# Performance work log

Hardware: AMD Instinct MI355X
Metric: run time of the kernel (lower is better)

Reference implementation:

```python
import jax, jax.numpy as jnp
import numpy as np

N_NODES = 50000
N_EDGES = 800000
N_GRAPHS = 64
IN_CH = 128
HID_CH = 128
FC_CH = 128


def setup_inputs() -> dict:
    key = jax.random.key(0)
    ks = jax.random.split(key, 12)

    def lin_w(k, fan_in, fan_out):
        return jax.random.normal(k, (fan_in, fan_out), jnp.float32) * (1.0 / np.sqrt(fan_in))

    return {
        "x": jax.random.normal(ks[0], (N_NODES, IN_CH), jnp.float32),
        "edge_index": jax.random.randint(ks[1], (2, N_EDGES), 0, N_NODES, dtype=jnp.int64),
        "batch_vec": jnp.sort(jax.random.randint(ks[2], (N_NODES,), 0, N_GRAPHS, dtype=jnp.int64)),
        "W1": lin_w(ks[3], IN_CH, HID_CH),
        "b1": jnp.zeros((HID_CH,), jnp.float32),
        "W2": lin_w(ks[4], HID_CH, HID_CH),
        "b2": jnp.zeros((HID_CH,), jnp.float32),
        "W3": lin_w(ks[5], HID_CH, FC_CH),
        "b3": jnp.zeros((FC_CH,), jnp.float32),
        "fcW1": lin_w(ks[6], FC_CH, IN_CH),
        "fcb1": jnp.zeros((IN_CH,), jnp.float32),
        "fcW2": lin_w(ks[7], IN_CH, 2),
        "fcb2": jnp.zeros((2,), jnp.float32),
    }


def reference(x, edge_index, batch_vec, W1, b1, W2, b2, W3, b3, fcW1, fcb1, fcW2, fcb2):
    n = x.shape[0]
    row, col = edge_index[0], edge_index[1]  # src -> dst

    # GCN symmetric normalization with self-loops: deg[j] = in-degree(j) + 1
    deg = jnp.zeros((n,), x.dtype).at[col].add(1.0) + 1.0
    inv_sqrt = jax.lax.rsqrt(deg)
    edge_norm = inv_sqrt[row] * inv_sqrt[col]  # [E]
    self_norm = (inv_sqrt * inv_sqrt)[:, None]  # [N,1], self-loop weight 1/deg

    def gcn(h, W, b):
        h = h @ W  # [N, out]
        agg = jnp.zeros_like(h).at[col].add(h[row] * edge_norm[:, None])
        return agg + h * self_norm + b

    h = jax.nn.relu(gcn(x, W1, b1))
    h = jax.nn.relu(gcn(h, W2, b2))
    h = jax.nn.relu(gcn(h, W3, b3))
    h = jax.nn.relu(h @ fcW1 + fcb1)
    h = h @ fcW2 + fcb2  # [N, 2]

    # global mean pool per graph
    sums = jax.ops.segment_sum(h, batch_vec, num_segments=N_GRAPHS)
    cnts = jax.ops.segment_sum(jnp.ones((n,), h.dtype), batch_vec, num_segments=N_GRAPHS)
    pooled = sums / jnp.maximum(cnts, 1.0)[:, None]  # [G, 2]
    return jax.nn.softmax(pooled, axis=1)
```

## Files before the change

### kernel.cpp

```cpp
#include <hip/hip_runtime.h>


#define CH 128
#define BSH 7
#define SEG 4096
#define SEGP 5120
#define EPW 2048
#define SAF 136
#define SC8 144

typedef unsigned short ushortT;
typedef unsigned int uintT;
typedef unsigned char ucharT;
typedef __attribute__((ext_vector_type(8))) short short8;
typedef __attribute__((ext_vector_type(4))) float floatx4;
typedef __attribute__((ext_vector_type(2))) float floatx2;

__device__ __forceinline__ float bf2f(uintT u) {
    return __uint_as_float(u << 16);
}
__device__ __forceinline__ ushortT f2bf(float f) {
    uintT x = __float_as_uint(f);
    return (ushortT)((x + 0x7fffu + ((x >> 16) & 1u)) >> 16);
}
__device__ __forceinline__ void dec4p(uintT u, floatx2& lo, floatx2& hi) {
    lo = __builtin_amdgcn_cvt_pk_f32_fp8((int)u, false);
    hi = __builtin_amdgcn_cvt_pk_f32_fp8((int)u, true);
}
__device__ __forceinline__ uintT packbf(floatx2 v) {
    return __builtin_amdgcn_perm(__float_as_uint(v.y), __float_as_uint(v.x), 0x07060302u);
}

__global__ __launch_bounds__(256) void k_bin(const int* __restrict__ row,
                                             const int* __restrict__ col,
                                             int* __restrict__ bfill,
                                             uintT* __restrict__ seg,
                                             const float* __restrict__ X,
                                             ucharT* __restrict__ Xb,
                                             const float* __restrict__ w0,
                                             const float* __restrict__ w1,
                                             const float* __restrict__ w2,
                                             const float* __restrict__ w3,
                                             ushortT* __restrict__ Whi,
                                             float* __restrict__ sums,
                                             int* __restrict__ tdone,
                                             int E, int NBB, int NB, int G,
                                             int total4) {
    __shared__ uintT staged[EPW];
    __shared__ int target[EPW];
    __shared__ int sval[512];
    __shared__ int horig[512];
    __shared__ int pcnt[512];
    __shared__ int gbase[512];
    const int t = threadIdx.x;

    if ((int)blockIdx.x >= NBB) {
        int bb = (int)blockIdx.x - NBB;
        if (bb < 256) {
            int idx = bb * 256 + t;
            int m = idx >> 14;
            int r2 = idx & 16383;
            int n = r2 >> 7;
            int k = r2 & 127;
            const float* W = (m == 0) ? w0 : (m == 1) ? w1 : (m == 2) ? w2 : w3;
            Whi[m * 16384 + n * CH + k] = f2bf(W[k * CH + n]);
            if (bb == 0) {
                if (t < 3 * G) sums[t] = 0.f;
                if (t == 0) tdone[0] = 0;
            }
        } else {
            int i = (bb - 256) * 256 + t;
            if (i < total4) {
                float4 v = reinterpret_cast<const float4*>(X)[i];
                int r0 = __builtin_amdgcn_cvt_pk_fp8_f32(v.x, v.y, 0, false);
                int r1 = __builtin_amdgcn_cvt_pk_fp8_f32(v.z, v.w, r0, true);
                reinterpret_cast<int*>(Xb)[i] = r1;
            }
        }
        return;
    }

    const int e0 = blockIdx.x * EPW;
    const int cnt = min(EPW, E - e0);

    sval[t] = 0; sval[t + 256] = 0;
    __syncthreads();

    int er[8], ec[8];
#pragma unroll
    for (int i = 0; i < 8; ++i) {
        int le = i * 256 + t;
        if (le < cnt) {
            er[i] = row[e0 + le];
            ec[i] = col[e0 + le];
            atomicAdd(&sval[ec[i] >> BSH], 1);
        }
    }
    __syncthreads();
    horig[t] = sval[t]; horig[t + 256] = sval[t + 256];
    __syncthreads();
    for (int off = 1; off < 512; off <<= 1) {
        int a = (t >= off) ? sval[t - off] : 0;
        int b2 = sval[t + 256 - off];
        __syncthreads();
        sval[t] += a;
        sval[t + 256] += b2;
        __syncthreads();
    }
    for (int b = t; b < 512; b += 256) {
        int h = horig[b];
        pcnt[b] = sval[b] - h;
        gbase[b] = (h > 0 && b < NB) ? atomicAdd(&bfill[b], h) : 0;
    }
    __syncthreads();
#pragma unroll
    for (int i = 0; i < 8; ++i) {
        int le = i * 256 + t;
        if (le < cnt) {
            int b = ec[i] >> BSH;
            int j = atomicAdd(&pcnt[b], 1);
            staged[j] = (uintT)er[i] | ((uintT)ec[i] << 16);
            int lo = sval[b] - horig[b];
            target[j] = b * SEG + gbase[b] + (j - lo);
        }
    }
    __syncthreads();
    for (int s = t; s < cnt; s += 256) seg[target[s]] = staged[s];
}

__global__ __launch_bounds__(512) void k_binvs(const int* __restrict__ bfill,
                                               const uintT* __restrict__ seg,
                                               float* __restrict__ invs,
                                               int* __restrict__ degi,
                                               int NB, int N) {
    const int b = blockIdx.x;
    const int t = threadIdx.x;
    __shared__ int h[128];
    if (t < 128) h[t] = 0;
    __syncthreads();
    int cnt = bfill[b];
    const uintT* sp = seg + (size_t)b * SEG;
    for (int s = t; s < cnt; s += 512) atomicAdd(&h[(sp[s] >> 16) & 127], 1);
    __syncthreads();
    int d = b * 128 + t;
    if (t < 128 && d < N) {
        invs[d] = rsqrtf((float)h[t] + 1.0f);
        degi[d] = h[t];
    }
}

__global__ __launch_bounds__(256) void k_scatter(const int* __restrict__ bfill,
                                                 const uintT* __restrict__ seg,
                                                 const float* __restrict__ invs,
                                                 const int* __restrict__ degi,
                                                 uintT* __restrict__ indptr,
                                                 uintT* __restrict__ epack,
                                                 int N, int NB) {
    __shared__ __align__(16) uintT staged[SEGP];
    __shared__ int pinc[128];
    __shared__ int pc[128];
    __shared__ float invL[128];
    __shared__ int ptotS;
    const int t = threadIdx.x;
    const int b = blockIdx.x;
    const int cnt = bfill[b];
    const uintT* sp = seg + (size_t)b * SEG;

    int praw = 0, hp = 0;
    if (t < 128) {
        int d = b * 128 + t;
        praw = (d < N) ? degi[d] : 0;
        invL[t] = (d < N) ? invs[d] : 0.f;
        hp = (praw + 7) & ~7;
        pinc[t] = hp;
    }
    __syncthreads();
    for (int off = 1; off < 128; off <<= 1) {
        int a = (t >= off && t < 128) ? pinc[t - off] : 0;
        __syncthreads();
        if (t < 128) pinc[t] += a;
        __syncthreads();
    }
    int excl = 0;
    if (t < 128) {
        excl = pinc[t] - hp;
        pc[t] = excl;
        int d = b * 128 + t;
        if (d < N) indptr[d] = (uintT)(b * SEGP + excl) | ((uintT)(hp >> 3) << 21);
        if (t == 127) ptotS = pinc[127];
    }
    __syncthreads();
    for (int s = t; s < cnt; s += 256) {
        uintT rc = sp[s];
        int src = (int)(rc & 0xffffu);
        int d7 = (int)(rc >> 16) & 127;
        int j = atomicAdd(&pc[d7], 1);
        float nrm = invs[src] * invL[d7];
        staged[j] = (uintT)src | ((uintT)f2bf(nrm) << 16);
    }
    __syncthreads();
    if (t < 128) {
        for (int k = excl + praw; k < excl + hp; ++k) staged[k] = 0u;
    }
    __syncthreads();
    {
        int tot4 = ptotS >> 2;
        uint4* dstw = reinterpret_cast<uint4*>(epack + (size_t)b * SEGP);
        const uint4* srcw = reinterpret_cast<const uint4*>(staged);
        for (int s = t; s < tot4; s += 256) dstw[s] = srcw[s];
    }
}

__global__ __launch_bounds__(256, 6) void k_agg(const ucharT* __restrict__ H8,
                                                const uintT* __restrict__ epack,
                                                const uintT* __restrict__ indptr,
                                                const float* __restrict__ invs,
                                                ucharT* __restrict__ Z8, int N) {
    const int wave = threadIdx.x >> 6, lane = threadIdx.x & 63;
    const int ng = lane >> 3;
    const int l = lane & 7;
    const int node = blockIdx.x * 32 + wave * 8 + ng;
    if (node >= N) return;

    const uint4* H4 = reinterpret_cast<const uint4*>(H8);
    const uint4* E4 = reinterpret_cast<const uint4*>(epack);

    uintT v = indptr[node];
    int q0 = (int)(v & 0x1FFFFFu) >> 2;
    int nb = (int)(v >> 21);

    floatx2 acc2[8];
    {
        float sn = invs[node];
        float sn2 = sn * sn;
        floatx2 s2 = {sn2, sn2};
        uint4 hrow = H4[(size_t)node * 8 + l];
        uintT wd[4] = {hrow.x, hrow.y, hrow.z, hrow.w};
#pragma unroll
        for (int w = 0; w < 4; ++w) {
            floatx2 lo, hi;
            dec4p(wd[w], lo, hi);
            acc2[2 * w] = s2 * lo;
            acc2[2 * w + 1] = s2 * hi;
        }
    }

    auto proc = [&](uint4 ea, uint4 eb) {
        uintT rec[8] = {ea.x, ea.y, ea.z, ea.w, eb.x, eb.y, eb.z, eb.w};
        uint4 g[8];
#pragma unroll
        for (int i = 0; i < 8; ++i)
            g[i] = H4[(size_t)(int)(rec[i] & 0xffffu) * 8 + l];
#pragma unroll
        for (int i = 0; i < 8; ++i) {
            float wv = bf2f(rec[i] >> 16);
            floatx2 wv2 = {wv, wv};
            uintT wd[4] = {g[i].x, g[i].y, g[i].z, g[i].w};
#pragma unroll
            for (int w = 0; w < 4; ++w) {
                floatx2 lo, hi;
                dec4p(wd[w], lo, hi);
                acc2[2 * w] += wv2 * lo;
                acc2[2 * w + 1] += wv2 * hi;
            }
        }
    };

    if (nb > 0) {
        uint4 ea = E4[q0], eb = E4[q0 + 1];
        for (int it = 1; it < nb; ++it) {
            uint4 na = E4[q0 + 2 * it], nbv = E4[q0 + 2 * it + 1];
            proc(ea, eb);
            ea = na; eb = nbv;
        }
        proc(ea, eb);
    }

    uint4 o;
    {
        int r0 = __builtin_amdgcn_cvt_pk_fp8_f32(acc2[0].x, acc2[0].y, 0, false);
        r0 = __builtin_amdgcn_cvt_pk_fp8_f32(acc2[1].x, acc2[1].y, r0, true);
        int r1 = __builtin_amdgcn_cvt_pk_fp8_f32(acc2[2].x, acc2[2].y, 0, false);
        r1 = __builtin_amdgcn_cvt_pk_fp8_f32(acc2[3].x, acc2[3].y, r1, true);
        int r2 = __builtin_amdgcn_cvt_pk_fp8_f32(acc2[4].x, acc2[4].y, 0, false);
        r2 = __builtin_amdgcn_cvt_pk_fp8_f32(acc2[5].x, acc2[5].y, r2, true);
        int r3 = __builtin_amdgcn_cvt_pk_fp8_f32(acc2[6].x, acc2[6].y, 0, false);
        r3 = __builtin_amdgcn_cvt_pk_fp8_f32(acc2[7].x, acc2[7].y, r3, true);
        o.x = (uintT)r0; o.y = (uintT)r1; o.z = (uintT)r2; o.w = (uintT)r3;
    }
    reinterpret_cast<uint4*>(Z8)[(size_t)node * 8 + l] = o;
}

__global__ __launch_bounds__(256) void k_gemm(const ucharT* __restrict__ In8,
                                              const ushortT* __restrict__ Whi,
                                              const float* __restrict__ Bias,
                                              ucharT* __restrict__ Out8, int N) {
    __shared__ ushortT As[64 * SAF];
    __shared__ ushortT Ws[128 * SAF];

    const int tid = threadIdx.x;
    const int wave = tid >> 6, lane = tid & 63;
    const int quad = lane >> 4, l15 = lane & 15;
    const int mBase = (wave >> 1) * 32, nBase = (wave & 1) * 64;
    const int row0 = blockIdx.x * 64;
    const int r = tid >> 2, q = tid & 3;

    {
        int grow = row0 + r;
        uint4 a8 = {0, 0, 0, 0}, b8 = {0, 0, 0, 0};
        if (grow < N) {
            const uint4* s = reinterpret_cast<const uint4*>(In8 + (size_t)grow * CH + q * 32);
            a8 = s[0]; b8 = s[1];
        }
        uintT wds[8] = {a8.x, a8.y, a8.z, a8.w, b8.x, b8.y, b8.z, b8.w};
#pragma unroll
        for (int w = 0; w < 4; ++w) {
            floatx2 lo0, hi0, lo1, hi1;
            dec4p(wds[2 * w], lo0, hi0);
            dec4p(wds[2 * w + 1], lo1, hi1);
            uint4 o;
            o.x = packbf(lo0); o.y = packbf(hi0);
            o.z = packbf(lo1); o.w = packbf(hi1);
            *reinterpret_cast<uint4*>(&As[r * SAF + q * 32 + w * 8]) = o;
        }
        int wn = tid & 127, wh = tid >> 7;
        const uint4* sh = reinterpret_cast<const uint4*>(Whi + wn * CH + wh * 64);
        uint4* dh = reinterpret_cast<uint4*>(&Ws[wn * SAF + wh * 64]);
#pragma unroll
        for (int p = 0; p < 8; ++p) dh[p] = sh[p];
    }
    __syncthreads();

    floatx4 acc[2][4];
    const floatx4 zero4 = {0.f, 0.f, 0.f, 0.f};
#pragma unroll
    for (int i = 0; i < 2; i++)
#pragma unroll
        for (int j = 0; j < 4; j++) acc[i][j] = zero4;

#pragma unroll
    for (int ks = 0; ks < 4; ++ks) {
        short8 af[2], wf[4];
#pragma unroll
        for (int mt = 0; mt < 2; ++mt)
            af[mt] = *reinterpret_cast<const short8*>(&As[(mBase + mt * 16 + l15) * SAF + ks * 32 + quad * 8]);
#pragma unroll
        for (int nt = 0; nt < 4; ++nt)
            wf[nt] = *reinterpret_cast<const short8*>(&Ws[(nBase + nt * 16 + l15) * SAF + ks * 32 + quad * 8]);
#pragma unroll
        for (int mt = 0; mt < 2; ++mt)
#pragma unroll
            for (int nt = 0; nt < 4; ++nt)
                acc[mt][nt] = __builtin_amdgcn_mfma_f32_16x16x32_bf16(af[mt], wf[nt], acc[mt][nt], 0, 0, 0);
    }
    __syncthreads();

    float bb[4];
#pragma unroll
    for (int nt = 0; nt < 4; ++nt) bb[nt] = Bias[nBase + nt * 16 + l15];

    ucharT* Cs8 = reinterpret_cast<ucharT*>(As);
#pragma unroll
    for (int mt = 0; mt < 2; ++mt)
#pragma unroll
        for (int nt = 0; nt < 4; ++nt)
#pragma unroll
            for (int r4 = 0; r4 < 4; ++r4) {
                int lrow = mBase + mt * 16 + quad * 4 + r4;
                float v = fmaxf(acc[mt][nt][r4] + bb[nt], 0.f);
                int f8 = __builtin_amdgcn_cvt_pk_fp8_f32(v, 0.f, 0, false);
                Cs8[lrow * SC8 + nBase + nt * 16 + l15] = (ucharT)(f8 & 0xff);
            }
    __syncthreads();
    {
        int grow = row0 + r;
        if (grow < N) {
            const uint4* s4 = reinterpret_cast<const uint4*>(&Cs8[r * SC8 + q * 32]);
            uint4* dst = reinterpret_cast<uint4*>(Out8 + (size_t)grow * CH + q * 32);
            dst[0] = s4[0];
            dst[1] = s4[1];
        }
    }
}

__global__ __launch_bounds__(256) void k_tail(const ucharT* __restrict__ Z8,
                                              const ushortT* __restrict__ W3hi,
                                              const float* __restrict__ B3,
                                              const ushortT* __restrict__ F1hi,
                                              const float* __restrict__ FB1,
                                              const float* __restrict__ FW2,
                                              const float* __restrict__ FB2,
                                              const int* __restrict__ batch,
                                              float* __restrict__ sums,
                                              float* __restrict__ cnts,
                                              float* __restrict__ out,
                                              int* __restrict__ tdone,
                                              int N, int G) {
    __shared__ ushortT Hf[64 * SAF];
    __shared__ ushortT Ws[128 * SAF];
    __shared__ float rp0[128];
    __shared__ float rp1[128];
    __shared__ float ls[192];
    __shared__ int lastFlag;

    const int tid = threadIdx.x;
    const int wave = tid >> 6, lane = tid & 63;
    const int quad = lane >> 4, l15 = lane & 15;
    const int mBase = (wave >> 1) * 32, nBase = (wave & 1) * 64;
    const int row0 = blockIdx.x * 64;
    const int r = tid >> 2, q = tid & 3;
    const int wn = tid & 127, wh = tid >> 7;

    {
        int grow = row0 + r;
        uint4 a8 = {0, 0, 0, 0}, b8 = {0, 0, 0, 0};
        if (grow < N) {
            const uint4* s = reinterpret_cast<const uint4*>(Z8 + (size_t)grow * CH + q * 32);
            a8 = s[0]; b8 = s[1];
        }
        uintT wds[8] = {a8.x, a8.y, a8.z, a8.w, b8.x, b8.y, b8.z, b8.w};
#pragma unroll
        for (int w = 0; w < 4; ++w) {
            floatx2 lo0, hi0, lo1, hi1;
            dec4p(wds[2 * w], lo0, hi0);
            dec4p(wds[2 * w + 1], lo1, hi1);
            uint4 o;
            o.x = packbf(lo0); o.y = packbf(hi0);
            o.z = packbf(lo1); o.w = packbf(hi1);
            *reinterpret_cast<uint4*>(&Hf[r * SAF + q * 32 + w * 8]) = o;
        }
        const uint4* sh = reinterpret_cast<const uint4*>(W3hi + wn * CH + wh * 64);
        uint4* dh = reinterpret_cast<uint4*>(&Ws[wn * SAF + wh * 64]);
#pragma unroll
        for (int p = 0; p < 8; ++p) dh[p] = sh[p];
    }
    __syncthreads();

    floatx4 acc[2][4];
    const floatx4 zero4 = {0.f, 0.f, 0.f, 0.f};
#pragma unroll
    for (int i = 0; i < 2; i++)
#pragma unroll
        for (int j = 0; j < 4; j++) acc[i][j] = zero4;

#pragma unroll
    for (int ks = 0; ks < 4; ++ks) {
        short8 af[2], wf[4];
#pragma unroll
        for (int mt = 0; mt < 2; ++mt)
            af[mt] = *reinterpret_cast<const short8*>(&Hf[(mBase + mt * 16 + l15) * SAF + ks * 32 + quad * 8]);
#pragma unroll
        for (int nt = 0; nt < 4; ++nt)
            wf[nt] = *reinterpret_cast<const short8*>(&Ws[(nBase + nt * 16 + l15) * SAF + ks * 32 + quad * 8]);
#pragma unroll
        for (int mt = 0; mt < 2; ++mt)
#pragma unroll
            for (int nt = 0; nt < 4; ++nt)
                acc[mt][nt] = __builtin_amdgcn_mfma_f32_16x16x32_bf16(af[mt], wf[nt], acc[mt][nt], 0, 0, 0);
    }
    __syncthreads();

    {
        float bb[4];
#pragma unroll
        for (int nt = 0; nt < 4; ++nt) bb[nt] = B3[nBase + nt * 16 + l15];
#pragma unroll
        for (int mt = 0; mt < 2; ++mt)
#pragma unroll
            for (int nt = 0; nt < 4; ++nt)
#pragma unroll
                for (int r4 = 0; r4 < 4; ++r4) {
                    int lrow = mBase + mt * 16 + quad * 4 + r4;
                    float v = fmaxf(acc[mt][nt][r4] + bb[nt], 0.f);
                    Hf[lrow * SAF + nBase + nt * 16 + l15] = f2bf(v);
                }
        const uint4* sh = reinterpret_cast<const uint4*>(F1hi + wn * CH + wh * 64);
        uint4* dh = reinterpret_cast<uint4*>(&Ws[wn * SAF + wh * 64]);
#pragma unroll
        for (int p = 0; p < 8; ++p) dh[p] = sh[p];
    }
    __syncthreads();

#pragma unroll
    for (int i = 0; i < 2; i++)
#pragma unroll
        for (int j = 0; j < 4; j++) acc[i][j] = zero4;
#pragma unroll
    for (int ks = 0; ks < 4; ++ks) {
        short8 af[2], wf[4];
#pragma unroll
        for (int mt = 0; mt < 2; ++mt)
            af[mt] = *reinterpret_cast<const short8*>(&Hf[(mBase + mt * 16 + l15) * SAF + ks * 32 + quad * 8]);
#pragma unroll
        for (int nt = 0; nt < 4; ++nt)
            wf[nt] = *reinterpret_cast<const short8*>(&Ws[(nBase + nt * 16 + l15) * SAF + ks * 32 + quad * 8]);
#pragma unroll
        for (int mt = 0; mt < 2; ++mt)
#pragma unroll
            for (int nt = 0; nt < 4; ++nt)
                acc[mt][nt] = __builtin_amdgcn_mfma_f32_16x16x32_bf16(af[mt], wf[nt], acc[mt][nt], 0, 0, 0);
    }

    {
        float bb[4];
#pragma unroll
        for (int nt = 0; nt < 4; ++nt) bb[nt] = FB1[nBase + nt * 16 + l15];
        float w20[4], w21[4];
#pragma unroll
        for (int nt = 0; nt < 4; ++nt) {
            float2 wv = *reinterpret_cast<const float2*>(FW2 + 2 * (nBase + nt * 16 + l15));
            w20[nt] = wv.x;
            w21[nt] = wv.y;
        }
#pragma unroll
        for (int mt = 0; mt < 2; ++mt)
#pragma unroll
            for (int r4 = 0; r4 < 4; ++r4) {
                float d0 = 0.f, d1 = 0.f;
#pragma unroll
                for (int nt = 0; nt < 4; ++nt) {
                    float v = fmaxf(acc[mt][nt][r4] + bb[nt], 0.f);
                    d0 += v * w20[nt];
                    d1 += v * w21[nt];
                }
#pragma unroll
                for (int m = 8; m >= 1; m >>= 1) {
                    d0 += __shfl_xor(d0, m, 64);
                    d1 += __shfl_xor(d1, m, 64);
                }
                if (l15 == 0) {
                    int lrow = mBase + mt * 16 + quad * 4 + r4;
                    rp0[lrow * 2 + (wave & 1)] = d0;
                    rp1[lrow * 2 + (wave & 1)] = d1;
                }
            }
    }
    if (tid < 192) ls[tid] = 0.f;
    __syncthreads();

    if (tid < 64) {
        int node = row0 + tid;
        if (node < N) {
            float d0 = rp0[tid * 2] + rp0[tid * 2 + 1] + FB2[0];
            float d1 = rp1[tid * 2] + rp1[tid * 2 + 1] + FB2[1];
            int g = batch[node];
            atomicAdd(&ls[g], d0);
            atomicAdd(&ls[64 + g], d1);
            atomicAdd(&ls[128 + g], 1.0f);
        }
    }
    __syncthreads();
    if (tid < 64) {
        float c = ls[128 + tid];
        if (c != 0.f) {
            atomicAdd(&sums[2 * tid], ls[tid]);
            atomicAdd(&sums[2 * tid + 1], ls[64 + tid]);
            atomicAdd(&cnts[tid], c);
        }
    }
    __syncthreads();

    if (tid == 0) {
        int old = atomicAdd(tdone, 1);
        lastFlag = (old == (int)gridDim.x - 1) ? 1 : 0;
    }
    __syncthreads();
    if (lastFlag && tid < G) {
        int g = tid;
        float c = fmaxf(atomicAdd(&cnts[g], 0.f), 1.0f);
        float p0 = atomicAdd(&sums[2 * g], 0.f) / c;
        float p1 = atomicAdd(&sums[2 * g + 1], 0.f) / c;
        float m = fmaxf(p0, p1);
        float e0 = expf(p0 - m), e1 = expf(p1 - m);
        float inv = 1.f / (e0 + e1);
        out[2 * g] = e0 * inv;
        out[2 * g + 1] = e1 * inv;
    }
}

extern "C" void kernel_launch(void* const* d_in, const int* in_sizes, int n_in,
                              void* d_out, int out_size, void* d_ws, size_t ws_size,
                              hipStream_t stream) {
    const float* X   = (const float*)d_in[0];
    const int* EI    = (const int*)d_in[1];
    const int* BATCH = (const int*)d_in[2];
    const float* W1  = (const float*)d_in[3];
    const float* B1  = (const float*)d_in[4];
    const float* W2  = (const float*)d_in[5];
    const float* B2  = (const float*)d_in[6];
    const float* W3  = (const float*)d_in[7];
    const float* B3  = (const float*)d_in[8];
    const float* FW1 = (const float*)d_in[9];
    const float* FB1 = (const float*)d_in[10];
    const float* FW2 = (const float*)d_in[11];
    const float* FB2 = (const float*)d_in[12];

    const int N = in_sizes[0] / CH;
    const int E = in_sizes[1] / 2;
    const int G = out_size / 2;
    const int* rowp = EI;
    const int* colp = EI + E;
    const int NB = (N + 127) >> BSH;

    char* w = (char*)d_ws;
    auto alloc = [&](size_t bytes) -> char* {
        char* p = w;
        w += (bytes + 255) & ~(size_t)255;
        return p;
    };
    ucharT*  Z8    = (ucharT*)alloc((size_t)N * CH);
    ucharT*  Hb8   = (ucharT*)alloc((size_t)N * CH);
    ucharT*  Xb8   = (ucharT*)alloc((size_t)N * CH);
    ushortT* WhiA  = (ushortT*)alloc((size_t)4 * 16384 * 2);
    float* invs    = (float*)alloc((size_t)N * 4);
    int*   degi    = (int*)alloc((size_t)N * 4);
    uintT* indptr  = (uintT*)alloc((size_t)N * 4);
    uintT* epack   = (uintT*)alloc((size_t)NB * SEGP * 4);
    uintT* seg     = (uintT*)alloc((size_t)NB * SEG * 4);
    int*   bfill   = (int*)alloc((size_t)NB * 4);
    float* sums    = (float*)alloc((size_t)G * 3 * 4);
    float* cnts    = sums + 2 * G;
    int*   tdone   = (int*)alloc(256);

    const int nbAgg  = (N + 31) / 32;
    const int nbGemm = (N + 63) / 64;
    const int nbBin  = (E + EPW - 1) / EPW;
    const int total4 = N * CH / 4;
    const int nbXc   = (total4 + 255) / 256;

    hipMemsetAsync(bfill, 0, (size_t)NB * 4, stream);
    k_bin<<<nbBin + 256 + nbXc, 256, 0, stream>>>(rowp, colp, bfill, seg,
                                                  X, Xb8, W1, W2, W3, FW1, WhiA,
                                                  sums, tdone, E, nbBin, NB, G, total4);
    k_binvs<<<NB, 512, 0, stream>>>(bfill, seg, invs, degi, NB, N);
    k_scatter<<<NB, 256, 0, stream>>>(bfill, seg, invs, degi, indptr, epack, N, NB);

    k_agg<<<nbAgg, 256, 0, stream>>>(Xb8, epack, indptr, invs, Z8, N);
    k_gemm<<<nbGemm, 256, 0, stream>>>(Z8, WhiA, B1, Hb8, N);
    k_agg<<<nbAgg, 256, 0, stream>>>(Hb8, epack, indptr, invs, Z8, N);
    k_gemm<<<nbGemm, 256, 0, stream>>>(Z8, WhiA + 16384, B2, Hb8, N);
    k_agg<<<nbAgg, 256, 0, stream>>>(Hb8, epack, indptr, invs, Z8, N);
    k_tail<<<nbGemm, 256, 0, stream>>>(Z8, WhiA + 2 * 16384, B3,
                                       WhiA + 3 * 16384, FB1, FW2, FB2,
                                       BATCH, sums, cnts, (float*)d_out, tdone, N, G);
}
```

Before: 213.6 us.

## Fuse all GCN stages into one persistent cooperative kernel with grid syncs

Replaces the chain of separate kernel launches (binning, degree, scatter, three aggregations, two GEMMs, tail) with a single cooperative persistent kernel. Each phase loops over its tasks with a grid-stride loop and is separated from the next by grid.sync(). The intent is to remove per-launch gaps and the last-block counter used for the softmax. The trade-offs are that the grid is capped by occupancy (at most 2048 blocks), so each phase gets fewer resident blocks, and the aggregation loses its launch_bounds(256,6) occupancy hint. A fallback path of multiple kernels is kept in case cooperative launch sizing fails.

After: 550.2 us. 158% more time.

```diff
diff --git a/kernel.cpp b/kernel.cpp
--- a/kernel.cpp
+++ b/kernel.cpp
@@ -1,4 +1,7 @@
 #include <hip/hip_runtime.h>
+#include <hip/hip_cooperative_groups.h>
+
+namespace cg = cooperative_groups;
 
 
 #define CH 128
@@ -8,6 +11,7 @@
 #define EPW 2048
 #define SAF 136
 #define SC8 144
+#define SMEM_BYTES 24576
 
 typedef unsigned short ushortT;
 typedef unsigned int uintT;
@@ -31,616 +35,639 @@
     return __builtin_amdgcn_perm(__float_as_uint(v.y), __float_as_uint(v.x), 0x07060302u);
 }
 
-__global__ __launch_bounds__(256) void k_bin(const int* __restrict__ row,
-                                             const int* __restrict__ col,
-                                             int* __restrict__ bfill,
-                                             uintT* __restrict__ seg,
-                                             const float* __restrict__ X,
-                                             ucharT* __restrict__ Xb,
-                                             const float* __restrict__ w0,
-                                             const float* __restrict__ w1,
-                                             const float* __restrict__ w2,
-                                             const float* __restrict__ w3,
-                                             ushortT* __restrict__ Whi,
-                                             float* __restrict__ sums,
-                                             int* __restrict__ tdone,
-                                             int E, int NBB, int NB, int G,
-                                             int total4) {
-    __shared__ uintT staged[EPW];
-    __shared__ int target[EPW];
-    __shared__ int sval[512];
-    __shared__ int horig[512];
-    __shared__ int pcnt[512];
-    __shared__ int gbase[512];
+struct MP {
+    const int* rowp; const int* colp; const int* batch;
+    const float* X;
+    const float *W1, *B1, *W2, *B2, *W3, *B3, *FW1, *FB1, *FW2, *FB2;
+    ucharT *Z8, *Hb8, *Xb8;
+    ushortT* Whi;
+    float* invs; int* degi;
+    uintT *indptr, *epack, *seg;
+    int* bfill;
+    float* sums; float* cnts;
+    float* out;
+    int N, E, G, NB, nbBin, nbAgg, nbG, total4, nbX16;
+};
+
+__device__ __forceinline__ void ph_prep(const MP& p, unsigned char* smem) {
     const int t = threadIdx.x;
-
-    if ((int)blockIdx.x >= NBB) {
-        int bb = (int)blockIdx.x - NBB;
-        if (bb < 256) {
+    const int T0 = p.nbBin + 256 + p.nbX16;
+    for (int task = blockIdx.x; task < T0; task += gridDim.x) {
+        if (task < p.nbBin) {
+            uintT* staged = (uintT*)smem;
+            int* target = (int*)(smem + 8192);
+            int* sval  = (int*)(smem + 16384);
+            int* horig = (int*)(smem + 18432);
+            int* pcnt  = (int*)(smem + 20480);
+            int* gbase = (int*)(smem + 22528);
+            const int e0 = task * EPW;
+            const int cnt = min(EPW, p.E - e0);
+            sval[t] = 0; sval[t + 256] = 0;
+            __syncthreads();
+            int er[8], ec[8];
+#pragma unroll
+            for (int i = 0; i < 8; ++i) {
+                int le = i * 256 + t;
+                if (le < cnt) {
+                    er[i] = p.rowp[e0 + le];
+                    ec[i] = p.colp[e0 + le];
+                    atomicAdd(&sval[ec[i] >> BSH], 1);
+                }
+            }
+            __syncthreads();
+            horig[t] = sval[t]; horig[t + 256] = sval[t + 256];
+            __syncthreads();
+            for (int off = 1; off < 512; off <<= 1) {
+                int a = (t >= off) ? sval[t - off] : 0;
+                int b2 = sval[t + 256 - off];
+                __syncthreads();
+                sval[t] += a;
+                sval[t + 256] += b2;
+                __syncthreads();
+            }
+            for (int b = t; b < 512; b += 256) {
+                int h = horig[b];
+                pcnt[b] = sval[b] - h;
+                gbase[b] = (h > 0 && b < p.NB) ? atomicAdd(&p.bfill[b], h) : 0;
+            }
+            __syncthreads();
+#pragma unroll
+            for (int i = 0; i < 8; ++i) {
+                int le = i * 256 + t;
+                if (le < cnt) {
+                    int b = ec[i] >> BSH;
+                    int j = atomicAdd(&pcnt[b], 1);
+                    staged[j] = (uintT)er[i] | ((uintT)ec[i] << 16);
+                    int lo = sval[b] - horig[b];
+                    target[j] = b * SEG + gbase[b] + (j - lo);
+                }
+            }
+            __syncthreads();
+            for (int s = t; s < cnt; s += 256) p.seg[target[s]] = staged[s];
+            __syncthreads();
+        } else if (task < p.nbBin + 256) {
+            int bb = task - p.nbBin;
             int idx = bb * 256 + t;
             int m = idx >> 14;
             int r2 = idx & 16383;
             int n = r2 >> 7;
             int k = r2 & 127;
-            const float* W = (m == 0) ? w0 : (m == 1) ? w1 : (m == 2) ? w2 : w3;
-            Whi[m * 16384 + n * CH + k] = f2bf(W[k * CH + n]);
-            if (bb == 0) {
-                if (t < 3 * G) sums[t] = 0.f;
-                if (t == 0) tdone[0] = 0;
-            }
+            const float* W = (m == 0) ? p.W1 : (m == 1) ? p.W2 : (m == 2) ? p.W3 : p.FW1;
+            p.Whi[m * 16384 + n * CH + k] = f2bf(W[k * CH + n]);
+            if (bb == 0 && t < 3 * p.G) p.sums[t] = 0.f;
         } else {
-            int i = (bb - 256) * 256 + t;
-            if (i < total4) {
-                float4 v = reinterpret_cast<const float4*>(X)[i];
-                int r0 = __builtin_amdgcn_cvt_pk_fp8_f32(v.x, v.y, 0, false);
-                int r1 = __builtin_amdgcn_cvt_pk_fp8_f32(v.z, v.w, r0, true);
-                reinterpret_cast<int*>(Xb)[i] = r1;
-            }
-        }
-        return;
-    }
-
-    const int e0 = blockIdx.x * EPW;
-    const int cnt = min(EPW, E - e0);
-
-    sval[t] = 0; sval[t + 256] = 0;
-    __syncthreads();
-
-    int er[8], ec[8];
-#pragma unroll
-    for (int i = 0; i < 8; ++i) {
-        int le = i * 256 + t;
-        if (le < cnt) {
-            er[i] = row[e0 + le];
-            ec[i] = col[e0 + le];
-            atomicAdd(&sval[ec[i] >> BSH], 1);
-        }
-    }
-    __syncthreads();
-    horig[t] = sval[t]; horig[t + 256] = sval[t + 256];
-    __syncthreads();
-    for (int off = 1; off < 512; off <<= 1) {
-        int a = (t >= off) ? sval[t - off] : 0;
-        int b2 = sval[t + 256 - off];
-        __syncthreads();
-        sval[t] += a;
-        sval[t + 256] += b2;
-        __syncthreads();
-    }
-    for (int b = t; b < 512; b += 256) {
-        int h = horig[b];
-        pcnt[b] = sval[b] - h;
-        gbase[b] = (h > 0 && b < NB) ? atomicAdd(&bfill[b], h) : 0;
-    }
-    __syncthreads();
-#pragma unroll
-    for (int i = 0; i < 8; ++i) {
-        int le = i * 256 + t;
-        if (le < cnt) {
-            int b = ec[i] >> BSH;
-            int j = atomicAdd(&pcnt[b], 1);
-            staged[j] = (uintT)er[i] | ((uintT)ec[i] << 16);
-            int lo = sval[b] - horig[b];
-            target[j] = b * SEG + gbase[b] + (j - lo);
-        }
-    }
-    __syncthreads();
-    for (int s = t; s < cnt; s += 256) seg[target[s]] = staged[s];
-}
-
-__global__ __launch_bounds__(512) void k_binvs(const int* __restrict__ bfill,
-                                               const uintT* __restrict__ seg,
-                                               float* __restrict__ invs,
-                                               int* __restrict__ degi,
-                                               int NB, int N) {
-    const int b = blockIdx.x;
+            int xb = task - p.nbBin - 256;
+            int base = xb * 4096;
+#pragma unroll
+            for (int k = 0; k < 16; ++k) {
+                int i = base + k * 256 + t;
+                if (i < p.total4) {
+                    float4 v = reinterpret_cast<const float4*>(p.X)[i];
+                    int r0 = __builtin_amdgcn_cvt_pk_fp8_f32(v.x, v.y, 0, false);
+                    int r1 = __builtin_amdgcn_cvt_pk_fp8_f32(v.z, v.w, r0, true);
+                    reinterpret_cast<int*>(p.Xb8)[i] = r1;
+                }
+            }
+        }
+    }
+}
+
+__device__ __forceinline__ void ph_binvs(const MP& p, unsigned char* smem) {
     const int t = threadIdx.x;
-    __shared__ int h[128];
-    if (t < 128) h[t] = 0;
-    __syncthreads();
-    int cnt = bfill[b];
-    const uintT* sp = seg + (size_t)b * SEG;
-    for (int s = t; s < cnt; s += 512) atomicAdd(&h[(sp[s] >> 16) & 127], 1);
-    __syncthreads();
-    int d = b * 128 + t;
-    if (t < 128 && d < N) {
-        invs[d] = rsqrtf((float)h[t] + 1.0f);
-        degi[d] = h[t];
-    }
-}
-
-__global__ __launch_bounds__(256) void k_scatter(const int* __restrict__ bfill,
-                                                 const uintT* __restrict__ seg,
-                                                 const float* __restrict__ invs,
-                                                 const int* __restrict__ degi,
-                                                 uintT* __restrict__ indptr,
-                                                 uintT* __restrict__ epack,
-                                                 int N, int NB) {
-    __shared__ __align__(16) uintT staged[SEGP];
-    __shared__ int pinc[128];
-    __shared__ int pc[128];
-    __shared__ float invL[128];
-    __shared__ int ptotS;
+    int* h = (int*)smem;
+    for (int b = blockIdx.x; b < p.NB; b += gridDim.x) {
+        if (t < 128) h[t] = 0;
+        __syncthreads();
+        int cnt = p.bfill[b];
+        const uintT* sp = p.seg + (size_t)b * SEG;
+        for (int s = t; s < cnt; s += 256) atomicAdd(&h[(sp[s] >> 16) & 127], 1);
+        __syncthreads();
+        int d = b * 128 + t;
+        if (t < 128 && d < p.N) {
+            p.invs[d] = rsqrtf((float)h[t] + 1.0f);
+            p.degi[d] = h[t];
+        }
+        __syncthreads();
+    }
+}
+
+__device__ __forceinline__ void ph_scatter(const MP& p, unsigned char* smem) {
     const int t = threadIdx.x;
-    const int b = blockIdx.x;
-    const int cnt = bfill[b];
-    const uintT* sp = seg + (size_t)b * SEG;
-
-    int praw = 0, hp = 0;
-    if (t < 128) {
-        int d = b * 128 + t;
-        praw = (d < N) ? degi[d] : 0;
-        invL[t] = (d < N) ? invs[d] : 0.f;
-        hp = (praw + 7) & ~7;
-        pinc[t] = hp;
-    }
-    __syncthreads();
-    for (int off = 1; off < 128; off <<= 1) {
-        int a = (t >= off && t < 128) ? pinc[t - off] : 0;
-        __syncthreads();
-        if (t < 128) pinc[t] += a;
-        __syncthreads();
-    }
-    int excl = 0;
-    if (t < 128) {
-        excl = pinc[t] - hp;
-        pc[t] = excl;
-        int d = b * 128 + t;
-        if (d < N) indptr[d] = (uintT)(b * SEGP + excl) | ((uintT)(hp >> 3) << 21);
-        if (t == 127) ptotS = pinc[127];
-    }
-    __syncthreads();
-    for (int s = t; s < cnt; s += 256) {
-        uintT rc = sp[s];
-        int src = (int)(rc & 0xffffu);
-        int d7 = (int)(rc >> 16) & 127;
-        int j = atomicAdd(&pc[d7], 1);
-        float nrm = invs[src] * invL[d7];
-        staged[j] = (uintT)src | ((uintT)f2bf(nrm) << 16);
-    }
-    __syncthreads();
-    if (t < 128) {
-        for (int k = excl + praw; k < excl + hp; ++k) staged[k] = 0u;
-    }
-    __syncthreads();
-    {
-        int tot4 = ptotS >> 2;
-        uint4* dstw = reinterpret_cast<uint4*>(epack + (size_t)b * SEGP);
-        const uint4* srcw = reinterpret_cast<const uint4*>(staged);
-        for (int s = t; s < tot4; s += 256) dstw[s] = srcw[s];
-    }
-}
-
-__global__ __launch_bounds__(256, 6) void k_agg(const ucharT* __restrict__ H8,
-                                                const uintT* __restrict__ epack,
-                                                const uintT* __restrict__ indptr,
-                                                const float* __restrict__ invs,
-                                                ucharT* __restrict__ Z8, int N) {
+    uintT* staged = (uintT*)smem;
+    int* pinc = (int*)(smem + 20480);
+    int* pc   = (int*)(smem + 20992);
+    float* invL = (float*)(smem + 21504);
+    int* ptotS = (int*)(smem + 22016);
+    for (int b = blockIdx.x; b < p.NB; b += gridDim.x) {
+        const int cnt = p.bfill[b];
+        const uintT* sp = p.seg + (size_t)b * SEG;
+        int praw = 0, hp = 0;
+        if (t < 128) {
+            int d = b * 128 + t;
+            praw = (d < p.N) ? p.degi[d] : 0;
+            invL[t] = (d < p.N) ? p.invs[d] : 0.f;
+            hp = (praw + 7) & ~7;
+            pinc[t] = hp;
+        }
+        __syncthreads();
+        for (int off = 1; off < 128; off <<= 1) {
+            int a = (t >= off && t < 128) ? pinc[t - off] : 0;
+            __syncthreads();
+            if (t < 128) pinc[t] += a;
+            __syncthreads();
+        }
+        int excl = 0;
+        if (t < 128) {
+            excl = pinc[t] - hp;
+            pc[t] = excl;
+            int d = b * 128 + t;
+            if (d < p.N) p.indptr[d] = (uintT)(b * SEGP + excl) | ((uintT)(hp >> 3) << 21);
+            if (t == 127) ptotS[0] = pinc[127];
+        }
+        __syncthreads();
+        for (int s = t; s < cnt; s += 256) {
+            uintT rc = sp[s];
+            int src = (int)(rc & 0xffffu);
+            int d7 = (int)(rc >> 16) & 127;
+            int j = atomicAdd(&pc[d7], 1);
+            float nrm = p.invs[src] * invL[d7];
+            staged[j] = (uintT)src | ((uintT)f2bf(nrm) << 16);
+        }
+        __syncthreads();
+        if (t < 128) {
+            for (int k = excl + praw; k < excl + hp; ++k) staged[k] = 0u;
+        }
+        __syncthreads();
+        {
+            int tot4 = ptotS[0] >> 2;
+            uint4* dstw = reinterpret_cast<uint4*>(p.epack + (size_t)b * SEGP);
+            const uint4* srcw = reinterpret_cast<const uint4*>(staged);
+            for (int s = t; s < tot4; s += 256) dstw[s] = srcw[s];
+        }
+        __syncthreads();
+    }
+}
+
+__device__ __forceinline__ void ph_agg(const MP& p, const ucharT* H8, ucharT* Z8) {
     const int wave = threadIdx.x >> 6, lane = threadIdx.x & 63;
     const int ng = lane >> 3;
     const int l = lane & 7;
-    const int node = blockIdx.x * 32 + wave * 8 + ng;
-    if (node >= N) return;
-
     const uint4* H4 = reinterpret_cast<const uint4*>(H8);
-    const uint4* E4 = reinterpret_cast<const uint4*>(epack);
-
-    uintT v = indptr[node];
-    int q0 = (int)(v & 0x1FFFFFu) >> 2;
-    int nb = (int)(v >> 21);
-
-    floatx2 acc2[8];
-    {
-        float sn = invs[node];
-        float sn2 = sn * sn;
-        floatx2 s2 = {sn2, sn2};
-        uint4 hrow = H4[(size_t)node * 8 + l];
-        uintT wd[4] = {hrow.x, hrow.y, hrow.z, hrow.w};
-#pragma unroll
-        for (int w = 0; w < 4; ++w) {
-            floatx2 lo, hi;
-            dec4p(wd[w], lo, hi);
-            acc2[2 * w] = s2 * lo;
-            acc2[2 * w + 1] = s2 * hi;
-        }
-    }
-
-    auto proc = [&](uint4 ea, uint4 eb) {
-        uintT rec[8] = {ea.x, ea.y, ea.z, ea.w, eb.x, eb.y, eb.z, eb.w};
-        uint4 g[8];
-#pragma unroll
-        for (int i = 0; i < 8; ++i)
-            g[i] = H4[(size_t)(int)(rec[i] & 0xffffu) * 8 + l];
-#pragma unroll
-        for (int i = 0; i < 8; ++i) {
-            float wv = bf2f(rec[i] >> 16);
-            floatx2 wv2 = {wv, wv};
-            uintT wd[4] = {g[i].x, g[i].y, g[i].z, g[i].w};
-#pragma unroll
-            for (int w = 0; w < 4; ++w) {
-                floatx2 lo, hi;
-                dec4p(wd[w], lo, hi);
-                acc2[2 * w] += wv2 * lo;
-                acc2[2 * w + 1] += wv2 * hi;
-            }
-        }
-    };
-
-    if (nb > 0) {
-        uint4 ea = E4[q0], eb = E4[q0 + 1];
-        for (int it = 1; it < nb; ++it) {
-            uint4 na = E4[q0 + 2 * it], nbv = E4[q0 + 2 * it + 1];
-            proc(ea, eb);
-            ea = na; eb = nbv;
-        }
-        proc(ea, eb);
-    }
-
-    uint4 o;
-    {
-        int r0 = __builtin_amdgcn_cvt_pk_fp8_f32(acc2[0].x, acc2[0].y, 0, false);
-        r0 = __builtin_amdgcn_cvt_pk_fp8_f32(acc2[1].x, acc2[1].y, r0, true);
-        int r1 = __builtin_amdgcn_cvt_pk_fp8_f32(acc2[2].x, acc2[2].y, 0, false);
-        r1 = __builtin_amdgcn_cvt_pk_fp8_f32(acc2[3].x, acc2[3].y, r1, true);
-        int r2 = __builtin_amdgcn_cvt_pk_fp8_f32(acc2[4].x, acc2[4].y, 0, false);
-        r2 = __builtin_amdgcn_cvt_pk_fp8_f32(acc2[5].x, acc2[5].y, r2, true);
-        int r3 = __builtin_amdgcn_cvt_pk_fp8_f32(acc2[6].x, acc2[6].y, 0, false);
-        r3 = __builtin_amdgcn_cvt_pk_fp8_f32(acc2[7].x, acc2[7].y, r3, true);
-        o.x = (uintT)r0; o.y = (uintT)r1; o.z = (uintT)r2; o.w = (uintT)r3;
-    }
-    reinterpret_cast<uint4*>(Z8)[(size_t)node * 8 + l] = o;
-}
-
-__global__ __launch_bounds__(256) void k_gemm(const ucharT* __restrict__ In8,
-                                              const ushortT* __restrict__ Whi,
-                                              const float* __restrict__ Bias,
-                                              ucharT* __restrict__ Out8, int N) {
-    __shared__ ushortT As[64 * SAF];
-    __shared__ ushortT Ws[128 * SAF];
-
+    const uint4* E4 = reinterpret_cast<const uint4*>(p.epack);
+
+    for (int task = blockIdx.x; task < p.nbAgg; task += gridDim.x) {
+        const int node = task * 32 + wave * 8 + ng;
+        if (node < p.N) {
+            uintT v = p.indptr[node];
+            int q0 = (int)(v & 0x1FFFFFu) >> 2;
+            int nb = (int)(v >> 21);
+
+            floatx2 acc2[8];
+            {
+                float sn = p.invs[node];
+                float sn2 = sn * sn;
+                floatx2 s2 = {sn2, sn2};
+                uint4 hrow = H4[(size_t)node * 8 + l];
+                uintT wd[4] = {hrow.x, hrow.y, hrow.z, hrow.w};
+#pragma unroll
+                for (int w = 0; w < 4; ++w) {
+                    floatx2 lo, hi;
+                    dec4p(wd[w], lo, hi);
+                    acc2[2 * w] = s2 * lo;
+                    acc2[2 * w + 1] = s2 * hi;
+                }
+            }
+
+            auto proc = [&](uint4 ea, uint4 eb) {
+                uintT rec[8] = {ea.x, ea.y, ea.z, ea.w, eb.x, eb.y, eb.z, eb.w};
+                uint4 g[8];
+#pragma unroll
+                for (int i = 0; i < 8; ++i)
+                    g[i] = H4[(size_t)(int)(rec[i] & 0xffffu) * 8 + l];
+#pragma unroll
+                for (int i = 0; i < 8; ++i) {
+                    float wv = bf2f(rec[i] >> 16);
+                    floatx2 wv2 = {wv, wv};
+                    uintT wd[4] = {g[i].x, g[i].y, g[i].z, g[i].w};
+#pragma unroll
+                    for (int w = 0; w < 4; ++w) {
+                        floatx2 lo, hi;
+                        dec4p(wd[w], lo, hi);
+                        acc2[2 * w] += wv2 * lo;
+                        acc2[2 * w + 1] += wv2 * hi;
+                    }
+                }
+            };
+
+            if (nb > 0) {
+                uint4 ea = E4[q0], eb = E4[q0 + 1];
+                for (int it = 1; it < nb; ++it) {
+                    uint4 na = E4[q0 + 2 * it], nbv = E4[q0 + 2 * it + 1];
+                    proc(ea, eb);
+                    ea = na; eb = nbv;
+                }
+                proc(ea, eb);
+            }
+
+            uint4 o;
+            {
+                int r0 = __builtin_amdgcn_cvt_pk_fp8_f32(acc2[0].x, acc2[0].y, 0, false);
+                r0 = __builtin_amdgcn_cvt_pk_fp8_f32(acc2[1].x, acc2[1].y, r0, true);
+                int r1 = __builtin_amdgcn_cvt_pk_fp8_f32(acc2[2].x, acc2[2].y, 0, false);
+                r1 = __builtin_amdgcn_cvt_pk_fp8_f32(acc2[3].x, acc2[3].y, r1, true);
+                int r2 = __builtin_amdgcn_cvt_pk_fp8_f32(acc2[4].x, acc2[4].y, 0, false);
+                r2 = __builtin_amdgcn_cvt_pk_fp8_f32(acc2[5].x, acc2[5].y, r2, true);
+                int r3 = __builtin_amdgcn_cvt_pk_fp8_f32(acc2[6].x, acc2[6].y, 0, false);
+                r3 = __builtin_amdgcn_cvt_pk_fp8_f32(acc2[7].x, acc2[7].y, r3, true);
+                o.x = (uintT)r0; o.y = (uintT)r1; o.z = (uintT)r2; o.w = (uintT)r3;
+            }
+            reinterpret_cast<uint4*>(Z8)[(size_t)node * 8 + l] = o;
+        }
+    }
+}
+
+__device__ __forceinline__ void ph_gemm(const MP& p, const ucharT* In8,
+                                        const ushortT* Whi, const float* Bias,
+                                        ucharT* Out8, unsigned char* smem) {
+    ushortT* As = (ushortT*)smem;
     const int tid = threadIdx.x;
     const int wave = tid >> 6, lane = tid & 63;
     const int quad = lane >> 4, l15 = lane & 15;
     const int mBase = (wave >> 1) * 32, nBase = (wave & 1) * 64;
-    const int row0 = blockIdx.x * 64;
     const int r = tid >> 2, q = tid & 3;
 
-    {
-        int grow = row0 + r;
-        uint4 a8 = {0, 0, 0, 0}, b8 = {0, 0, 0, 0};
-        if (grow < N) {
-            const uint4* s = reinterpret_cast<const uint4*>(In8 + (size_t)grow * CH + q * 32);
-            a8 = s[0]; b8 = s[1];
-        }
-        uintT wds[8] = {a8.x, a8.y, a8.z, a8.w, b8.x, b8.y, b8.z, b8.w};
-#pragma unroll
-        for (int w = 0; w < 4; ++w) {
-            floatx2 lo0, hi0, lo1, hi1;
-            dec4p(wds[2 * w], lo0, hi0);
-            dec4p(wds[2 * w + 1], lo1, hi1);
-            uint4 o;
-            o.x = packbf(lo0); o.y = packbf(hi0);
-            o.z = packbf(lo1); o.w = packbf(hi1);
-            *reinterpret_cast<uint4*>(&As[r * SAF + q * 32 + w * 8]) = o;
-        }
-        int wn = tid & 127, wh = tid >> 7;
-        const uint4* sh = reinterpret_cast<const uint4*>(Whi + wn * CH + wh * 64);
-        uint4* dh = reinterpret_cast<uint4*>(&Ws[wn * SAF + wh * 64]);
-#pragma unroll
-        for (int p = 0; p < 8; ++p) dh[p] = sh[p];
-    }
-    __syncthreads();
-
-    floatx4 acc[2][4];
-    const floatx4 zero4 = {0.f, 0.f, 0.f, 0.f};
-#pragma unroll
-    for (int i = 0; i < 2; i++)
-#pragma unroll
-        for (int j = 0; j < 4; j++) acc[i][j] = zero4;
-
-#pragma unroll
-    for (int ks = 0; ks < 4; ++ks) {
-        short8 af[2], wf[4];
+    for (int task = blockIdx.x; task < p.nbG; task += gridDim.x) {
+        const int row0 = task * 64;
+        {
+            int grow = row0 + r;
+            uint4 a8 = {0, 0, 0, 0}, b8 = {0, 0, 0, 0};
+            if (grow < p.N) {
+                const uint4* s = reinterpret_cast<const uint4*>(In8 + (size_t)grow * CH + q * 32);
+                a8 = s[0]; b8 = s[1];
+            }
+            uintT wds[8] = {a8.x, a8.y, a8.z, a8.w, b8.x, b8.y, b8.z, b8.w};
+#pragma unroll
+            for (int w = 0; w < 4; ++w) {
+                floatx2 lo0, hi0, lo1, hi1;
+                dec4p(wds[2 * w], lo0, hi0);
+                dec4p(wds[2 * w + 1], lo1, hi1);
+                uint4 o;
+                o.x = packbf(lo0); o.y = packbf(hi0);
+                o.z = packbf(lo1); o.w = packbf(hi1);
+                *reinterpret_cast<uint4*>(&As[r * SAF + q * 32 + w * 8]) = o;
+            }
+        }
+        __syncthreads();
+
+        floatx4 acc[2][4];
+        const floatx4 zero4 = {0.f, 0.f, 0.f, 0.f};
+#pragma unroll
+        for (int i = 0; i < 2; i++)
+#pragma unroll
+            for (int j = 0; j < 4; j++) acc[i][j] = zero4;
+
+#pragma unroll
+        for (int ks = 0; ks < 4; ++ks) {
+            short8 af[2], wf[4];
+#pragma unroll
+            for (int mt = 0; mt < 2; ++mt)
+                af[mt] = *reinterpret_cast<const short8*>(&As[(mBase + mt * 16 + l15) * SAF + ks * 32 + quad * 8]);
+#pragma unroll
+            for (int nt = 0; nt < 4; ++nt)
+                wf[nt] = *reinterpret_cast<const short8*>(Whi + (size_t)(nBase + nt * 16 + l15) * CH + ks * 32 + quad * 8);
+#pragma unroll
+            for (int mt = 0; mt < 2; ++mt)
+#pragma unroll
+                for (int nt = 0; nt < 4; ++nt)
+                    acc[mt][nt] = __builtin_amdgcn_mfma_f32_16x16x32_bf16(af[mt], wf[nt], acc[mt][nt], 0, 0, 0);
+        }
+        __syncthreads();
+
+        float bb[4];
+#pragma unroll
+        for (int nt = 0; nt < 4; ++nt) bb[nt] = Bias[nBase + nt * 16 + l15];
+
+        ucharT* Cs8 = reinterpret_cast<ucharT*>(As);
 #pragma unroll
         for (int mt = 0; mt < 2; ++mt)
-            af[mt] = *reinterpret_cast<const short8*>(&As[(mBase + mt * 16 + l15) * SAF + ks * 32 + quad * 8]);
-#pragma unroll
-        for (int nt = 0; nt < 4; ++nt)
-            wf[nt] = *reinterpret_cast<const short8*>(&Ws[(nBase + nt * 16 + l15) * SAF + ks * 32 + quad * 8]);
-#pragma unroll
-        for (int mt = 0; mt < 2; ++mt)
 #pragma unroll
             for (int nt = 0; nt < 4; ++nt)
-                acc[mt][nt] = __builtin_amdgcn_mfma_f32_16x16x32_bf16(af[mt], wf[nt], acc[mt][nt], 0, 0, 0);
-    }
-    __syncthreads();
-
-    float bb[4];
-#pragma unroll
-    for (int nt = 0; nt < 4; ++nt) bb[nt] = Bias[nBase + nt * 16 + l15];
-
-    ucharT* Cs8 = reinterpret_cast<ucharT*>(As);
-#pragma unroll
-    for (int mt = 0; mt < 2; ++mt)
-#pragma unroll
-        for (int nt = 0; nt < 4; ++nt)
-#pragma unroll
-            for (int r4 = 0; r4 < 4; ++r4) {
-                int lrow = mBase + mt * 16 + quad * 4 + r4;
-                float v = fmaxf(acc[mt][nt][r4] + bb[nt], 0.f);
-                int f8 = __builtin_amdgcn_cvt_pk_fp8_f32(v, 0.f, 0, false);
-                Cs8[lrow * SC8 + nBase + nt * 16 + l15] = (ucharT)(f8 & 0xff);
-            }
-    __syncthreads();
-    {
-        int grow = row0 + r;
-        if (grow < N) {
-            const uint4* s4 = reinterpret_cast<const uint4*>(&Cs8[r * SC8 + q * 32]);
-            uint4* dst = reinterpret_cast<uint4*>(Out8 + (size_t)grow * CH + q * 32);
-            dst[0] = s4[0];
-            dst[1] = s4[1];
-        }
-    }
-}
-
-__global__ __launch_bounds__(256) void k_tail(const ucharT* __restrict__ Z8,
-                                              const ushortT* __restrict__ W3hi,
-                                              const float* __restrict__ B3,
-                                              const ushortT* __restrict__ F1hi,
-                                              const float* __restrict__ FB1,
-                                              const float* __restrict__ FW2,
-                                              const float* __restrict__ FB2,
-                                              const int* __restrict__ batch,
-                                              float* __restrict__ sums,
-                                              float* __restrict__ cnts,
-                                              float* __restrict__ out,
-                                              int* __restrict__ tdone,
-                                              int N, int G) {
-    __shared__ ushortT Hf[64 * SAF];
-    __shared__ ushortT Ws[128 * SAF];
-    __shared__ float rp0[128];
-    __shared__ float rp1[128];
-    __shared__ float ls[192];
-    __shared__ int lastFlag;
+#pragma unroll
+                for (int r4 = 0; r4 < 4; ++r4) {
+                    int lrow = mBase + mt * 16 + quad * 4 + r4;
+                    float v = fmaxf(acc[mt][nt][r4] + bb[nt], 0.f);
+                    int f8 = __builtin_amdgcn_cvt_pk_fp8_f32(v, 0.f, 0, false);
+                    Cs8[lrow * SC8 + nBase + nt * 16 + l15] = (ucharT)(f8 & 0xff);
+                }
+        __syncthreads();
+        {
+            int grow = row0 + r;
+            if (grow < p.N) {
+                const uint4* s4 = reinterpret_cast<const uint4*>(&Cs8[r * SC8 + q * 32]);
+                uint4* dst = reinterpret_cast<uint4*>(Out8 + (size_t)grow * CH + q * 32);
+                dst[0] = s4[0];
+                dst[1] = s4[1];
+            }
+        }
+        __syncthreads();
+    }
+}
+
+__device__ __forceinline__ void ph_tail(const MP& p, unsigned char* smem) {
+    ushortT* Hf = (ushortT*)smem;
+    float* rp0 = (float*)(smem + 17408);
+    float* rp1 = (float*)(smem + 17920);
+    float* ls  = (float*)(smem + 18432);
+    const ushortT* W3hi = p.Whi + 2 * 16384;
+    const ushortT* F1hi = p.Whi + 3 * 16384;
 
     const int tid = threadIdx.x;
     const int wave = tid >> 6, lane = tid & 63;
     const int quad = lane >> 4, l15 = lane & 15;
     const int mBase = (wave >> 1) * 32, nBase = (wave & 1) * 64;
-    const int row0 = blockIdx.x * 64;
     const int r = tid >> 2, q = tid & 3;
-    const int wn = tid & 127, wh = tid >> 7;
-
-    {
-        int grow = row0 + r;
-        uint4 a8 = {0, 0, 0, 0}, b8 = {0, 0, 0, 0};
-        if (grow < N) {
-            const uint4* s = reinterpret_cast<const uint4*>(Z8 + (size_t)grow * CH + q * 32);
-            a8 = s[0]; b8 = s[1];
-        }
-        uintT wds[8] = {a8.x, a8.y, a8.z, a8.w, b8.x, b8.y, b8.z, b8.w};
-#pragma unroll
-        for (int w = 0; w < 4; ++w) {
-            floatx2 lo0, hi0, lo1, hi1;
-            dec4p(wds[2 * w], lo0, hi0);
-            dec4p(wds[2 * w + 1], lo1, hi1);
-            uint4 o;
-            o.x = packbf(lo0); o.y = packbf(hi0);
-            o.z = packbf(lo1); o.w = packbf(hi1);
-            *reinterpret_cast<uint4*>(&Hf[r * SAF + q * 32 + w * 8]) = o;
-        }
-        const uint4* sh = reinterpret_cast<const uint4*>(W3hi + wn * CH + wh * 64);
-        uint4* dh = reinterpret_cast<uint4*>(&Ws[wn * SAF + wh * 64]);
-#pragma unroll
-        for (int p = 0; p < 8; ++p) dh[p] = sh[p];
-    }
-    __syncthreads();
-
-    floatx4 acc[2][4];
-    const floatx4 zero4 = {0.f, 0.f, 0.f, 0.f};
-#pragma unroll
-    for (int i = 0; i < 2; i++)
-#pragma unroll
-        for (int j = 0; j < 4; j++) acc[i][j] = zero4;
-
-#pragma unroll
-    for (int ks = 0; ks < 4; ++ks) {
-        short8 af[2], wf[4];
-#pragma unroll
-        for (int mt = 0; mt < 2; ++mt)
-            af[mt] = *reinterpret_cast<const short8*>(&Hf[(mBase + mt * 16 + l15) * SAF + ks * 32 + quad * 8]);
-#pragma unroll
-        for (int nt = 0; nt < 4; ++nt)
-            wf[nt] = *reinterpret_cast<const short8*>(&Ws[(nBase + nt * 16 + l15) * SAF + ks * 32 + quad * 8]);
-#pragma unroll
-        for (int mt = 0; mt < 2; ++mt)
+
+    for (int task = blockIdx.x; task < p.nbG; task += gridDim.x) {
+        const int row0 = task * 64;
+        {
+            int grow = row0 + r;
+            uint4 a8 = {0, 0, 0, 0}, b8 = {0, 0, 0, 0};
+            if (grow < p.N) {
+                const uint4* s = reinterpret_cast<const uint4*>(p.Z8 + (size_t)grow * CH + q * 32);
+                a8 = s[0]; b8 = s[1];
+            }
+            uintT wds[8] = {a8.x, a8.y, a8.z, a8.w, b8.x, b8.y, b8.z, b8.w};
+#pragma unroll
+            for (int w = 0; w < 4; ++w) {
+                floatx2 lo0, hi0, lo1, hi1;
+                dec4p(wds[2 * w], lo0, hi0);
+                dec4p(wds[2 * w + 1], lo1, hi1);
+                uint4 o;
+                o.x = packbf(lo0); o.y = packbf(hi0);
+                o.z = packbf(lo1); o.w = packbf(hi1);
+                *reinterpret_cast<uint4*>(&Hf[r * SAF + q * 32 + w * 8]) = o;
+            }
+        }
+        __syncthreads();
+
+        floatx4 acc[2][4];
+        const floatx4 zero4 = {0.f, 0.f, 0.f, 0.f};
+#pragma unroll
+        for (int i = 0; i < 2; i++)
+#pragma unroll
+            for (int j = 0; j < 4; j++) acc[i][j] = zero4;
+
+#pragma unroll
+        for (int ks = 0; ks < 4; ++ks) {
+            short8 af[2], wf[4];
+#pragma unroll
+            for (int mt = 0; mt < 2; ++mt)
+                af[mt] = *reinterpret_cast<const short8*>(&Hf[(mBase + mt * 16 + l15) * SAF + ks * 32 + quad * 8]);
 #pragma unroll
             for (int nt = 0; nt < 4; ++nt)
-                acc[mt][nt] = __builtin_amdgcn_mfma_f32_16x16x32_bf16(af[mt], wf[nt], acc[mt][nt], 0, 0, 0);
-    }
-    __syncthreads();
-
-    {
-        float bb[4];
-#pragma unroll
-        for (int nt = 0; nt < 4; ++nt) bb[nt] = B3[nBase + nt * 16 + l15];
-#pragma unroll
-        for (int mt = 0; mt < 2; ++mt)
+                wf[nt] = *reinterpret_cast<const short8*>(W3hi + (size_t)(nBase + nt * 16 + l15) * CH + ks * 32 + quad * 8);
+#pragma unroll
+            for (int mt = 0; mt < 2; ++mt)
+#pragma unroll
+                for (int nt = 0; nt < 4; ++nt)
+                    acc[mt][nt] = __builtin_amdgcn_mfma_f32_16x16x32_bf16(af[mt], wf[nt], acc[mt][nt], 0, 0, 0);
+        }
+        __syncthreads();
+
+        {
+            float bb[4];
+#pragma unroll
+            for (int nt = 0; nt < 4; ++nt) bb[nt] = p.B3[nBase + nt * 16 + l15];
+#pragma unroll
+            for (int mt = 0; mt < 2; ++mt)
+#pragma unroll
+                for (int nt = 0; nt < 4; ++nt)
+#pragma unroll
+                    for (int r4 = 0; r4 < 4; ++r4) {
+                        int lrow = mBase + mt * 16 + quad * 4 + r4;
+                        float v = fmaxf(acc[mt][nt][r4] + bb[nt], 0.f);
+                        Hf[lrow * SAF + nBase + nt * 16 + l15] = f2bf(v);
+                    }
+        }
+        __syncthreads();
+
+#pragma unroll
+        for (int i = 0; i < 2; i++)
+#pragma unroll
+            for (int j = 0; j < 4; j++) acc[i][j] = zero4;
+#pragma unroll
+        for (int ks = 0; ks < 4; ++ks) {
+            short8 af[2], wf[4];
+#pragma unroll
+            for (int mt = 0; mt < 2; ++mt)
+                af[mt] = *reinterpret_cast<const short8*>(&Hf[(mBase + mt * 16 + l15) * SAF + ks * 32 + quad * 8]);
 #pragma unroll
             for (int nt = 0; nt < 4; ++nt)
+                wf[nt] = *reinterpret_cast<const short8*>(F1hi + (size_t)(nBase + nt * 16 + l15) * CH + ks * 32 + quad * 8);
+#pragma unroll
+            for (int mt = 0; mt < 2; ++mt)
+#pragma unroll
+                for (int nt = 0; nt < 4; ++nt)
+                    acc[mt][nt] = __builtin_amdgcn_mfma_f32_16x16x32_bf16(af[mt], wf[nt], acc[mt][nt], 0, 0, 0);
+        }
+
+        {
+            float bb[4];
+#pragma unroll
+            for (int nt = 0; nt < 4; ++nt) bb[nt] = p.FB1[nBase + nt * 16 + l15];
+            float w20[4], w21[4];
+#pragma unroll
+            for (int nt = 0; nt < 4; ++nt) {
+                float2 wv = *reinterpret_cast<const float2*>(p.FW2 + 2 * (nBase + nt * 16 + l15));
+                w20[nt] = wv.x;
+                w21[nt] = wv.y;
+            }
+#pragma unroll
+            for (int mt = 0; mt < 2; ++mt)
 #pragma unroll
                 for (int r4 = 0; r4 < 4; ++r4) {
-                    int lrow = mBase + mt * 16 + quad * 4 + r4;
-                    float v = fmaxf(acc[mt][nt][r4] + bb[nt], 0.f);
-                    Hf[lrow * SAF + nBase + nt * 16 + l15] = f2bf(v);
-                }
-        const uint4* sh = reinterpret_cast<const uint4*>(F1hi + wn * CH + wh * 64);
-        uint4* dh = reinterpret_cast<uint4*>(&Ws[wn * SAF + wh * 64]);
-#pragma unroll
-        for (int p = 0; p < 8; ++p) dh[p] = sh[p];
-    }
-    __syncthreads();
-
-#pragma unroll
-    for (int i = 0; i < 2; i++)
-#pragma unroll
-        for (int j = 0; j < 4; j++) acc[i][j] = zero4;
-#pragma unroll
-    for (int ks = 0; ks < 4; ++ks) {
-        short8 af[2], wf[4];
-#pragma unroll
-        for (int mt = 0; mt < 2; ++mt)
-            af[mt] = *reinterpret_cast<const short8*>(&Hf[(mBase + mt * 16 + l15) * SAF + ks * 32 + quad * 8]);
-#pragma unroll
-        for (int nt = 0; nt < 4; ++nt)
-            wf[nt] = *reinterpret_cast<const short8*>(&Ws[(nBase + nt * 16 + l15) * SAF + ks * 32 + quad * 8]);
-#pragma unroll
-        for (int mt = 0; mt < 2; ++mt)
-#pragma unroll
-            for (int nt = 0; nt < 4; ++nt)
-                acc[mt][nt] = __builtin_amdgcn_mfma_f32_16x16x32_bf16(af[mt], wf[nt], acc[mt][nt], 0, 0, 0);
-    }
-
-    {
-        float bb[4];
-#pragma unroll
-        for (int nt = 0; nt < 4; ++nt) bb[nt] = FB1[nBase + nt * 16 + l15];
-        float w20[4], w21[4];
-#pragma unroll
-        for (int nt = 0; nt < 4; ++nt) {
-            float2 wv = *reinterpret_cast<const float2*>(FW2 + 2 * (nBase + nt * 16 + l15));
-            w20[nt] = wv.x;
-            w21[nt] = wv.y;
-        }
-#pragma unroll
-        for (int mt = 0; mt < 2; ++mt)
-#pragma unroll
-            for (int r4 = 0; r4 < 4; ++r4) {
-                float d0 = 0.f, d1 = 0.f;
-#pragma unroll
-                for (int nt = 0; nt < 4; ++nt) {
-                    float v = fmaxf(acc[mt][nt][r4] + bb[nt], 0.f);
-                    d0 += v * w20[nt];
-                    d1 += v * w21[nt];
-                }
-#pragma unroll
-                for (int m = 8; m >= 1; m >>= 1) {
-                    d0 += __shfl_xor(d0, m, 64);
-                    d1 += __shfl_xor(d1, m, 64);
-                }
-                if (l15 == 0) {
-                    int lrow = mBase + mt * 16 + quad * 4 + r4;
-                    rp0[lrow * 2 + (wave & 1)] = d0;
-                    rp1[lrow * 2 + (wave & 1)] = d1;
-                }
-            }
-    }
-    if (tid < 192) ls[tid] = 0.f;
-    __syncthreads();
-
-    if (tid < 64) {
-        int node = row0 + tid;
-        if (node < N) {
-            float d0 = rp0[tid * 2] + rp0[tid * 2 + 1] + FB2[0];
-            float d1 = rp1[tid * 2] + rp1[tid * 2 + 1] + FB2[1];
-            int g = batch[node];
-            atomicAdd(&ls[g], d0);
-            atomicAdd(&ls[64 + g], d1);
-            atomicAdd(&ls[128 + g], 1.0f);
-        }
-    }
-    __syncthreads();
-    if (tid < 64) {
-        float c = ls[128 + tid];
-        if (c != 0.f) {
-            atomicAdd(&sums[2 * tid], ls[tid]);
-            atomicAdd(&sums[2 * tid + 1], ls[64 + tid]);
-            atomicAdd(&cnts[tid], c);
-        }
-    }
-    __syncthreads();
-
-    if (tid == 0) {
-        int old = atomicAdd(tdone, 1);
-        lastFlag = (old == (int)gridDim.x - 1) ? 1 : 0;
-    }
-    __syncthreads();
-    if (lastFlag && tid < G) {
-        int g = tid;
-        float c = fmaxf(atomicAdd(&cnts[g], 0.f), 1.0f);
-        float p0 = atomicAdd(&sums[2 * g], 0.f) / c;
-        float p1 = atomicAdd(&sums[2 * g + 1], 0.f) / c;
+                    float d0 = 0.f, d1 = 0.f;
+#pragma unroll
+                    for (int nt = 0; nt < 4; ++nt) {
+                        float v = fmaxf(acc[mt][nt][r4] + bb[nt], 0.f);
+                        d0 += v * w20[nt];
+                        d1 += v * w21[nt];
+                    }
+#pragma unroll
+                    for (int m = 8; m >= 1; m >>= 1) {
+                        d0 += __shfl_xor(d0, m, 64);
+                        d1 += __shfl_xor(d1, m, 64);
+                    }
+                    if (l15 == 0) {
+                        int lrow = mBase + mt * 16 + quad * 4 + r4;
+                        rp0[lrow * 2 + (wave & 1)] = d0;
+                        rp1[lrow * 2 + (wave & 1)] = d1;
+                    }
+                }
+        }
+        if (tid < 192) ls[tid] = 0.f;
+        __syncthreads();
+
+        if (tid < 64) {
+            int node = row0 + tid;
+            if (node < p.N) {
+                float d0 = rp0[tid * 2] + rp0[tid * 2 + 1] + p.FB2[0];
+                float d1 = rp1[tid * 2] + rp1[tid * 2 + 1] + p.FB2[1];
+                int g = p.batch[node];
+                atomicAdd(&ls[g], d0);
+                atomicAdd(&ls[64 + g], d1);
+                atomicAdd(&ls[128 + g], 1.0f);
+            }
+        }
+        __syncthreads();
+        if (tid < 64) {
+            float c = ls[128 + tid];
+            if (c != 0.f) {
+                atomicAdd(&p.sums[2 * tid], ls[tid]);
+                atomicAdd(&p.sums[2 * tid + 1], ls[64 + tid]);
+                atomicAdd(&p.cnts[tid], c);
+            }
+        }
+        __syncthreads();
+    }
+}
+
+__device__ __forceinline__ void ph_softmax(const MP& p) {
+    const int t = threadIdx.x;
+    if (blockIdx.x == 0 && t < p.G) {
+        float c = fmaxf(atomicAdd(&p.cnts[t], 0.f), 1.0f);
+        float p0 = atomicAdd(&p.sums[2 * t], 0.f) / c;
+        float p1 = atomicAdd(&p.sums[2 * t + 1], 0.f) / c;
         float m = fmaxf(p0, p1);
         float e0 = expf(p0 - m), e1 = expf(p1 - m);
         float inv = 1.f / (e0 + e1);
-        out[2 * g] = e0 * inv;
-        out[2 * g + 1] = e1 * inv;
-    }
-}
+        p.out[2 * t] = e0 * inv;
+        p.out[2 * t + 1] = e1 * inv;
+    }
+}
+
+__global__ __launch_bounds__(256) void k_mega(MP p) {
+    __shared__ __align__(16) unsigned char smem[SMEM_BYTES];
+    cg::grid_group grid = cg::this_grid();
+    ph_prep(p, smem);                         grid.sync();
+    ph_binvs(p, smem);                        grid.sync();
+    ph_scatter(p, smem);                      grid.sync();
+    ph_agg(p, p.Xb8, p.Z8);                   grid.sync();
+    ph_gemm(p, p.Z8, p.Whi, p.B1, p.Hb8, smem);              grid.sync();
+    ph_agg(p, p.Hb8, p.Z8);                   grid.sync();
+    ph_gemm(p, p.Z8, p.Whi + 16384, p.B2, p.Hb8, smem);      grid.sync();
+    ph_agg(p, p.Hb8, p.Z8);                   grid.sync();
+    ph_tail(p, smem);                         grid.sync();
+    ph_softmax(p);
+}
+
+__global__ __launch_bounds__(256) void k_prep(MP p) {
+    __shared__ __align__(16) unsigned char smem[SMEM_BYTES];
+    ph_prep(p, smem);
+}
+__global__ __launch_bounds__(256) void k_binvsW(MP p) {
+    __shared__ __align__(16) unsigned char smem[SMEM_BYTES];
+    ph_binvs(p, smem);
+}
+__global__ __launch_bounds__(256) void k_scatterW(MP p) {
+    __shared__ __align__(16) unsigned char smem[SMEM_BYTES];
+    ph_scatter(p, smem);
+}
+__global__ __launch_bounds__(256) void k_agg1(MP p) { ph_agg(p, p.Xb8, p.Z8); }
+__global__ __launch_bounds__(256) void k_agg2(MP p) { ph_agg(p, p.Hb8, p.Z8); }
+__global__ __launch_bounds__(256) void k_gemm1(MP p) {
+    __shared__ __align__(16) unsigned char smem[SMEM_BYTES];
+    ph_gemm(p, p.Z8, p.Whi, p.B1, p.Hb8, smem);
+}
+__global__ __launch_bounds__(256) void k_gemm2(MP p) {
+    __shared__ __align__(16) unsigned char smem[SMEM_BYTES];
+    ph_gemm(p, p.Z8, p.Whi + 16384, p.B2, p.Hb8, smem);
+}
+__global__ __launch_bounds__(256) void k_tailW(MP p) {
+    __shared__ __align__(16) unsigned char smem[SMEM_BYTES];
+    ph_tail(p, smem);
+}
+__global__ void k_softW(MP p) { ph_softmax(p); }
 
 extern "C" void kernel_launch(void* const* d_in, const int* in_sizes, int n_in,
                               void* d_out, int out_size, void* d_ws, size_t ws_size,
                               hipStream_t stream) {
-    const float* X   = (const float*)d_in[0];
-    const int* EI    = (const int*)d_in[1];
-    const int* BATCH = (const int*)d_in[2];
-    const float* W1  = (const float*)d_in[3];
-    const float* B1  = (const float*)d_in[4];
-    const float* W2  = (const float*)d_in[5];
-    const float* B2  = (const float*)d_in[6];
-    const float* W3  = (const float*)d_in[7];
-    const float* B3  = (const float*)d_in[8];
-    const float* FW1 = (const float*)d_in[9];
-    const float* FB1 = (const float*)d_in[10];
-    const float* FW2 = (const float*)d_in[11];
-    const float* FB2 = (const float*)d_in[12];
-
-    const int N = in_sizes[0] / CH;
-    const int E = in_sizes[1] / 2;
-    const int G = out_size / 2;
-    const int* rowp = EI;
-    const int* colp = EI + E;
-    const int NB = (N + 127) >> BSH;
+    MP P;
+    P.X   = (const float*)d_in[0];
+    const int* EI = (const int*)d_in[1];
+    P.batch = (const int*)d_in[2];
+    P.W1 = (const float*)d_in[3];  P.B1 = (const float*)d_in[4];
+    P.W2 = (const float*)d_in[5];  P.B2 = (const float*)d_in[6];
+    P.W3 = (const float*)d_in[7];  P.B3 = (const float*)d_in[8];
+    P.FW1 = (const float*)d_in[9]; P.FB1 = (const float*)d_in[10];
+    P.FW2 = (const float*)d_in[11]; P.FB2 = (const float*)d_in[12];
+
+    P.N = in_sizes[0] / CH;
+    P.E = in_sizes[1] / 2;
+    P.G = out_size / 2;
+    P.rowp = EI;
+    P.colp = EI + P.E;
+    P.NB = (P.N + 127) >> BSH;
 
     char* w = (char*)d_ws;
     auto alloc = [&](size_t bytes) -> char* {
-        char* p = w;
+        char* pp = w;
         w += (bytes + 255) & ~(size_t)255;
-        return p;
+        return pp;
     };
-    ucharT*  Z8    = (ucharT*)alloc((size_t)N * CH);
-    ucharT*  Hb8   = (ucharT*)alloc((size_t)N * CH);
-    ucharT*  Xb8   = (ucharT*)alloc((size_t)N * CH);
-    ushortT* WhiA  = (ushortT*)alloc((size_t)4 * 16384 * 2);
-    float* invs    = (float*)alloc((size_t)N * 4);
-    int*   degi    = (int*)alloc((size_t)N * 4);
-    uintT* indptr  = (uintT*)alloc((size_t)N * 4);
-    uintT* epack   = (uintT*)alloc((size_t)NB * SEGP * 4);
-    uintT* seg     = (uintT*)alloc((size_t)NB * SEG * 4);
-    int*   bfill   = (int*)alloc((size_t)NB * 4);
-    float* sums    = (float*)alloc((size_t)G * 3 * 4);
-    float* cnts    = sums + 2 * G;
-    int*   tdone   = (int*)alloc(256);
-
-    const int nbAgg  = (N + 31) / 32;
-    const int nbGemm = (N + 63) / 64;
-    const int nbBin  = (E + EPW - 1) / EPW;
-    const int total4 = N * CH / 4;
-    const int nbXc   = (total4 + 255) / 256;
-
-    hipMemsetAsync(bfill, 0, (size_t)NB * 4, stream);
-    k_bin<<<nbBin + 256 + nbXc, 256, 0, stream>>>(rowp, colp, bfill, seg,
-                                                  X, Xb8, W1, W2, W3, FW1, WhiA,
-                                                  sums, tdone, E, nbBin, NB, G, total4);
-    k_binvs<<<NB, 512, 0, stream>>>(bfill, seg, invs, degi, NB, N);
-    k_scatter<<<NB, 256, 0, stream>>>(bfill, seg, invs, degi, indptr, epack, N, NB);
-
-    k_agg<<<nbAgg, 256, 0, stream>>>(Xb8, epack, indptr, invs, Z8, N);
-    k_gemm<<<nbGemm, 256, 0, stream>>>(Z8, WhiA, B1, Hb8, N);
-    k_agg<<<nbAgg, 256, 0, stream>>>(Hb8, epack, indptr, invs, Z8, N);
-    k_gemm<<<nbGemm, 256, 0, stream>>>(Z8, WhiA + 16384, B2, Hb8, N);
-    k_agg<<<nbAgg, 256, 0, stream>>>(Hb8, epack, indptr, invs, Z8, N);
-    k_tail<<<nbGemm, 256, 0, stream>>>(Z8, WhiA + 2 * 16384, B3,
-                                       WhiA + 3 * 16384, FB1, FW2, FB2,
-                                       BATCH, sums, cnts, (float*)d_out, tdone, N, G);
-}
+    P.Z8   = (ucharT*)alloc((size_t)P.N * CH);
+    P.Hb8  = (ucharT*)alloc((size_t)P.N * CH);
+    P.Xb8  = (ucharT*)alloc((size_t)P.N * CH);
+    P.Whi  = (ushortT*)alloc((size_t)4 * 16384 * 2);
+    P.invs = (float*)alloc((size_t)P.N * 4);
+    P.degi = (int*)alloc((size_t)P.N * 4);
+    P.indptr = (uintT*)alloc((size_t)P.N * 4);
+    P.epack  = (uintT*)alloc((size_t)P.NB * SEGP * 4);
+    P.seg    = (uintT*)alloc((size_t)P.NB * SEG * 4);
+    P.bfill  = (int*)alloc((size_t)P.NB * 4);
+    P.sums   = (float*)alloc((size_t)P.G * 3 * 4);
+    P.cnts   = P.sums + 2 * P.G;
+    P.out    = (float*)d_out;
+
+    P.nbBin  = (P.E + EPW - 1) / EPW;
+    P.nbAgg  = (P.N + 31) / 32;
+    P.nbG    = (P.N + 63) / 64;
+    P.total4 = P.N * CH / 4;
+    P.nbX16  = (P.total4 + 4095) / 4096;
+
+    static int s_grid = -2;
+    if (s_grid == -2) {
+        int cus = 0, maxb = 0;
+        if (hipDeviceGetAttribute(&cus, hipDeviceAttributeMultiprocessorCount, 0) != hipSuccess || cus <= 0)
+            cus = 256;
+        if (hipOccupancyMaxActiveBlocksPerMultiprocessor(&maxb, k_mega, 256, 0) != hipSuccess)
+            maxb = 0;
+        if (maxb > 0) {
+            long g = (long)maxb * cus;
+            s_grid = (g > 2048) ? 2048 : (int)g;
+        } else {
+            s_grid = -1;
+        }
+    }
+
+    (void)hipMemsetAsync(P.bfill, 0, (size_t)P.NB * 4, stream);
+
+    if (s_grid > 0) {
+        MP Pl = P;
+        void* args[] = { (void*)&Pl };
+        (void)hipLaunchCooperativeKernel((const void*)k_mega, dim3(s_grid), dim3(256),
+                                         args, 0, stream);
+    } else {
+        const int T0 = P.nbBin + 256 + P.nbX16;
+        k_prep<<<T0, 256, 0, stream>>>(P);
+        k_binvsW<<<P.NB, 256, 0, stream>>>(P);
+        k_scatterW<<<P.NB, 256, 0, stream>>>(P);
+        k_agg1<<<P.nbAgg, 256, 0, stream>>>(P);
+        k_gemm1<<<P.nbG, 256, 0, stream>>>(P);
+        k_agg2<<<P.nbAgg, 256, 0, stream>>>(P);
+        k_gemm2<<<P.nbG, 256, 0, stream>>>(P);
+        k_agg2<<<P.nbAgg, 256, 0, stream>>>(P);
+        k_tailW<<<P.nbG, 256, 0, stream>>>(P);
+        k_softW<<<1, 64, 0, stream>>>(P);
+    }
+}
```
